# Kernel optimization log

Hardware: AMD Instinct MI355X
Metric: run time of the kernel (lower is better)

The kernel has to match this reference:

```python
import jax, jax.numpy as jnp
import numpy as np
from jax import lax

D_MODEL = 768
N_LAYER = 4
VOCAB = 50280  # 50277 padded to multiple of 8
D_INNER = 2 * D_MODEL
D_STATE = 16
D_CONV = 4
DT_RANK = 48  # ceil(768/16)
EPS = 1e-5


def setup_inputs() -> dict:
    key = jax.random.key(0)
    ks = iter(jax.random.split(key, 16))
    s = 0.02
    B, L = 1, 1024
    inp = {
        "input_ids": jax.random.randint(next(ks), (B, L), 0, 50277, dtype=jnp.int64).astype(jnp.int32),
        "embedding": jax.random.normal(next(ks), (VOCAB, D_MODEL), jnp.float32) * s,
        "in_proj_w": jax.random.normal(next(ks), (N_LAYER, 2 * D_INNER, D_MODEL), jnp.float32) * s,
        "conv_w": jax.random.normal(next(ks), (N_LAYER, D_INNER, 1, D_CONV), jnp.float32) * s,
        "conv_b": jnp.zeros((N_LAYER, D_INNER), jnp.float32),
        "x_proj_w": jax.random.normal(next(ks), (N_LAYER, DT_RANK + 2 * D_STATE, D_INNER), jnp.float32) * s,
        "dt_proj_w": jax.random.normal(next(ks), (N_LAYER, D_INNER, DT_RANK), jnp.float32) * s,
        "dt_proj_b": jax.random.uniform(next(ks), (N_LAYER, D_INNER), jnp.float32, -4.0, -2.0),
        "A_log": jnp.log(jnp.broadcast_to(jnp.arange(1, D_STATE + 1, dtype=jnp.float32), (N_LAYER, D_INNER, D_STATE))),
        "D_param": jnp.ones((N_LAYER, D_INNER), jnp.float32),
        "out_proj_w": jax.random.normal(next(ks), (N_LAYER, D_MODEL, D_INNER), jnp.float32) * s,
        "norm_w": jnp.ones((N_LAYER, D_MODEL), jnp.float32),
        "norm_f_w": jnp.ones((D_MODEL,), jnp.float32),
    }
    return inp


def rmsnorm(x, w):
    var = jnp.mean(jnp.square(x), axis=-1, keepdims=True)
    return x * lax.rsqrt(var + EPS) * w


def silu(x):
    return x * jax.nn.sigmoid(x)


def mamba_mixer(h, in_w, cw, cb, xw, dtw, dtb, A_log, Dp, ow):
    B, L, _ = h.shape
    xz = jnp.einsum("bld,ed->ble", h, in_w)          # [B,L,2*d_inner]
    x, z = jnp.split(xz, 2, axis=-1)
    # causal depthwise conv1d over length
    xc = lax.conv_general_dilated(
        x.transpose(0, 2, 1), cw, (1,), [(D_CONV - 1, 0)],
        dimension_numbers=("NCH", "OIH", "NCH"), feature_group_count=D_INNER,
    ).transpose(0, 2, 1) + cb                          # [B,L,d_inner]
    xc = silu(xc)
    dbl = jnp.einsum("bld,ed->ble", xc, xw)            # [B,L,R+2N]
    dt = jax.nn.softplus(jnp.einsum("blr,dr->bld", dbl[..., :DT_RANK], dtw) + dtb)
    Bm = dbl[..., DT_RANK:DT_RANK + D_STATE]           # [B,L,N]
    Cm = dbl[..., DT_RANK + D_STATE:]                  # [B,L,N]
    A = -jnp.exp(A_log)                                # [d_inner,N]
    dA = jnp.exp(dt[..., None] * A)                    # [B,L,d_inner,N]
    dBx = dt[..., None] * Bm[:, :, None, :] * xc[..., None]

    def step(s, inp):
        a, b, c = inp
        s = a * s + b
        y = jnp.einsum("bdn,bn->bd", s, c)
        return s, y

    s0 = jnp.zeros((B, D_INNER, D_STATE), h.dtype)
    _, ys = lax.scan(step, s0, (dA.transpose(1, 0, 2, 3), dBx.transpose(1, 0, 2, 3), Cm.transpose(1, 0, 2)))
    y = ys.transpose(1, 0, 2) + xc * Dp                # [B,L,d_inner]
    y = y * silu(z)
    return jnp.einsum("ble,de->bld", y, ow)


def reference(input_ids, embedding, in_proj_w, conv_w, conv_b, x_proj_w,
              dt_proj_w, dt_proj_b, A_log, D_param, out_proj_w, norm_w, norm_f_w):
    h = embedding[input_ids]                           # [B,L,D]
    for i in range(N_LAYER):
        h = h + mamba_mixer(rmsnorm(h, norm_w[i]), in_proj_w[i], conv_w[i], conv_b[i],
                            x_proj_w[i], dt_proj_w[i], dt_proj_b[i], A_log[i],
                            D_param[i], out_proj_w[i])
    h = rmsnorm(h, norm_f_w)
    logits = jnp.einsum("bld,vd->blv", h, embedding)   # tied lm_head
    return logits
```

## Files before the change

### kernel.cpp

```cpp
#include <hip/hip_runtime.h>
#include <cstdint>
#include <cstddef>

#define N_LAYER 4
#define VOCABSZ 50280
#define VOCABPAD 50304
#define DMODEL 768
#define DINNER 1536
#define DSTATE 16
#define DTRANK 48
#define SEQL 1024

typedef __bf16 bf16x8 __attribute__((ext_vector_type(8)));
typedef unsigned short us8 __attribute__((ext_vector_type(8)));
typedef float f32x4 __attribute__((ext_vector_type(4)));

__device__ __forceinline__ unsigned short f2bf(float f) {
    unsigned int u = __builtin_bit_cast(unsigned int, f);
    u = (u + 0x7FFFu + ((u >> 16) & 1u)) >> 16;
    return (unsigned short)u;
}

__device__ __forceinline__ void glds16(const unsigned short* g, unsigned short* l) {
    __builtin_amdgcn_global_load_lds(
        (const __attribute__((address_space(1))) void*)g,
        (__attribute__((address_space(3))) void*)l, 16, 0, 0);
}

__global__ __launch_bounds__(256) void cvt_bf16_kernel(
    const float* __restrict__ src, unsigned short* __restrict__ dst, int n8)
{
    int i = blockIdx.x * 256 + threadIdx.x;
    if (i >= n8) return;
    const float4* s = (const float4*)src + (size_t)i * 2;
    float4 a = s[0], b = s[1];
    us8 o = { f2bf(a.x), f2bf(a.y), f2bf(a.z), f2bf(a.w),
              f2bf(b.x), f2bf(b.y), f2bf(b.z), f2bf(b.w) };
    *(us8*)(dst + (size_t)i * 8) = o;
}

__global__ __launch_bounds__(256) void cvt_xw_kernel(
    const float* __restrict__ xw, unsigned short* __restrict__ xwB)
{
    int g = blockIdx.x * 256 + threadIdx.x;
    if (g >= N_LAYER * 128 * 192) return;
    int row = g / 192;
    int c8  = g % 192;
    int layer = row >> 7;
    int r = row & 127;
    us8 o;
    if (r < 80) {
        const float4* s = (const float4*)(xw + ((size_t)(layer * 80 + r) * DINNER) + c8 * 8);
        float4 a = s[0], b = s[1];
        o = (us8){ f2bf(a.x), f2bf(a.y), f2bf(a.z), f2bf(a.w),
                   f2bf(b.x), f2bf(b.y), f2bf(b.z), f2bf(b.w) };
    } else {
        o = (us8){0, 0, 0, 0, 0, 0, 0, 0};
    }
    *(us8*)(xwB + (size_t)row * DINNER + c8 * 8) = o;
}

template <int ADD>
__device__ __forceinline__ void gemm_bf_body(
    const unsigned short* __restrict__ A, const unsigned short* __restrict__ B,
    const float* __restrict__ ADDSRC, float* __restrict__ C, int N, int K)
{
    __shared__ unsigned short sA[128 * 32];
    __shared__ unsigned short sB[128 * 32];

    const int tid  = threadIdx.x;
    const int lane = tid & 63;
    const int wave = tid >> 6;
    const int wm = (wave & 1) * 64;
    const int wn = (wave >> 1) * 64;
    const int bid = blockIdx.x;
    const int cpx = (int)gridDim.x >> 3;
    const int swz = (bid & 7) * cpx + (bid >> 3);
    const int bm = (swz & 7) << 7;
    const int bn = (swz >> 3) << 7;

    const unsigned short* Ag0 = A + (size_t)(bm + (tid >> 2)) * K + (tid & 3) * 8;
    const unsigned short* Ag1 = Ag0 + (size_t)64 * K;
    const unsigned short* Bg0 = B + (size_t)(bn + (tid >> 2)) * K + (tid & 3) * 8;
    const unsigned short* Bg1 = Bg0 + (size_t)64 * K;
    unsigned short* lA0 = sA + tid * 8;
    unsigned short* lA1 = lA0 + 2048;
    unsigned short* lB0 = sB + tid * 8;
    unsigned short* lB1 = lB0 + 2048;

    f32x4 acc[4][4];
#pragma unroll
    for (int i = 0; i < 4; ++i)
#pragma unroll
        for (int j = 0; j < 4; ++j) acc[i][j] = (f32x4){0.f, 0.f, 0.f, 0.f};

    const int fr = (lane & 15) * 32 + (lane >> 4) * 8;

    for (int k0 = 0; k0 < K; k0 += 32) {
        __syncthreads();
        glds16(Ag0, lA0);
        glds16(Ag1, lA1);
        glds16(Bg0, lB0);
        glds16(Bg1, lB1);
        Ag0 += 32; Ag1 += 32; Bg0 += 32; Bg1 += 32;
        __syncthreads();

        bf16x8 af[4], bfr[4];
#pragma unroll
        for (int t = 0; t < 4; ++t) {
            af[t]  = __builtin_bit_cast(bf16x8, *(const us8*)&sA[(wm + t * 16) * 32 + fr]);
            bfr[t] = __builtin_bit_cast(bf16x8, *(const us8*)&sB[(wn + t * 16) * 32 + fr]);
        }
#pragma unroll
        for (int mt = 0; mt < 4; ++mt)
#pragma unroll
            for (int nt = 0; nt < 4; ++nt)
                acc[mt][nt] = __builtin_amdgcn_mfma_f32_16x16x32_bf16(
                    af[mt], bfr[nt], acc[mt][nt], 0, 0, 0);
    }

    const int cn = lane & 15;
    const int cm = (lane >> 4) * 4;
#pragma unroll
    for (int mt = 0; mt < 4; ++mt) {
#pragma unroll
        for (int nt = 0; nt < 4; ++nt) {
            int n = bn + wn + nt * 16 + cn;
            if (n < N) {
#pragma unroll
                for (int r = 0; r < 4; ++r) {
                    int m = bm + wm + mt * 16 + cm + r;
                    size_t idx = (size_t)m * N + n;
                    float v = acc[mt][nt][r];
                    if constexpr (ADD) v += ADDSRC[idx];
                    C[idx] = v;
                }
            }
        }
    }
}

__global__ __launch_bounds__(256) void gemm_in_kernel(
    const unsigned short* __restrict__ A, const unsigned short* __restrict__ B,
    float* __restrict__ C, int N, int K)
{ gemm_bf_body<0>(A, B, nullptr, C, N, K); }

__global__ __launch_bounds__(256) void gemm_out_kernel(
    const unsigned short* __restrict__ A, const unsigned short* __restrict__ B,
    const float* __restrict__ ADDSRC, float* __restrict__ C, int N, int K)
{ gemm_bf_body<1>(A, B, ADDSRC, C, N, K); }

__global__ __launch_bounds__(256) void gemm_xproj_kernel(
    const unsigned short* __restrict__ A, const unsigned short* __restrict__ B,
    float* __restrict__ C, int N, int K)
{ gemm_bf_body<0>(A, B, nullptr, C, N, K); }

__global__ __launch_bounds__(256) void gemm_logits_kernel(
    const unsigned short* __restrict__ A, const unsigned short* __restrict__ B,
    float* __restrict__ C, int N, int K)
{ gemm_bf_body<0>(A, B, nullptr, C, N, K); }

template <int ADD>
__global__ __launch_bounds__(256) void gemm_fb_kernel(
    const float* __restrict__ A, const float* __restrict__ B,
    const float* __restrict__ ADDSRC, float* __restrict__ C,
    int N, int K)
{
    __shared__ unsigned short sA[128 * 40];
    __shared__ unsigned short sB[128 * 40];
    const int tid  = threadIdx.x;
    const int lane = tid & 63;
    const int wave = tid >> 6;
    const int wm = (wave & 1) * 64;
    const int wn = (wave >> 1) * 64;
    const int bm = blockIdx.y * 128;
    const int bn = blockIdx.x * 128;
    const int srow = tid >> 1;
    const int scol = (tid & 1) * 16;
    const float* Ap = A + (size_t)(bm + srow) * K + scol;
    const int brow  = bn + srow;
    const bool bvalid = brow < N;
    const float* Bp = B + (size_t)(bvalid ? brow : 0) * K + scol;
    f32x4 acc[4][4];
#pragma unroll
    for (int i = 0; i < 4; ++i)
#pragma unroll
        for (int j = 0; j < 4; ++j) acc[i][j] = (f32x4){0.f, 0.f, 0.f, 0.f};
    unsigned short* sAp = &sA[srow * 40 + scol];
    unsigned short* sBp = &sB[srow * 40 + scol];
    const int fr = (lane & 15) * 40 + (lane >> 4) * 8;
    for (int k0 = 0; k0 < K; k0 += 32) {
        float4 a0 = *(const float4*)(Ap + k0);
        float4 a1 = *(const float4*)(Ap + k0 + 4);
        float4 a2 = *(const float4*)(Ap + k0 + 8);
        float4 a3 = *(const float4*)(Ap + k0 + 12);
        float4 b0, b1, b2, b3;
        if (bvalid) {
            b0 = *(const float4*)(Bp + k0);
            b1 = *(const float4*)(Bp + k0 + 4);
            b2 = *(const float4*)(Bp + k0 + 8);
            b3 = *(const float4*)(Bp + k0 + 12);
        } else {
            b0 = make_float4(0.f, 0.f, 0.f, 0.f);
            b1 = b0; b2 = b0; b3 = b0;
        }
        __syncthreads();
        us8 va0 = { f2bf(a0.x), f2bf(a0.y), f2bf(a0.z), f2bf(a0.w),
                    f2bf(a1.x), f2bf(a1.y), f2bf(a1.z), f2bf(a1.w) };
        us8 va1 = { f2bf(a2.x), f2bf(a2.y), f2bf(a2.z), f2bf(a2.w),
                    f2bf(a3.x), f2bf(a3.y), f2bf(a3.z), f2bf(a3.w) };
        us8 vb0 = { f2bf(b0.x), f2bf(b0.y), f2bf(b0.z), f2bf(b0.w),
                    f2bf(b1.x), f2bf(b1.y), f2bf(b1.z), f2bf(b1.w) };
        us8 vb1 = { f2bf(b2.x), f2bf(b2.y), f2bf(b2.z), f2bf(b2.w),
                    f2bf(b3.x), f2bf(b3.y), f2bf(b3.z), f2bf(b3.w) };
        *(us8*)(sAp)     = va0;
        *(us8*)(sAp + 8) = va1;
        *(us8*)(sBp)     = vb0;
        *(us8*)(sBp + 8) = vb1;
        __syncthreads();
        bf16x8 af[4], bfr[4];
#pragma unroll
        for (int t = 0; t < 4; ++t) {
            af[t]  = __builtin_bit_cast(bf16x8, *(const us8*)&sA[wm * 40 + t * 640 + fr]);
            bfr[t] = __builtin_bit_cast(bf16x8, *(const us8*)&sB[wn * 40 + t * 640 + fr]);
        }
#pragma unroll
        for (int mt = 0; mt < 4; ++mt)
#pragma unroll
            for (int nt = 0; nt < 4; ++nt)
                acc[mt][nt] = __builtin_amdgcn_mfma_f32_16x16x32_bf16(
                    af[mt], bfr[nt], acc[mt][nt], 0, 0, 0);
    }
    const int cn = lane & 15;
    const int cm = (lane >> 4) * 4;
#pragma unroll
    for (int mt = 0; mt < 4; ++mt) {
#pragma unroll
        for (int nt = 0; nt < 4; ++nt) {
            int n = bn + wn + nt * 16 + cn;
            if (n < N) {
#pragma unroll
                for (int r = 0; r < 4; ++r) {
                    int m = bm + wm + mt * 16 + cm + r;
                    size_t idx = (size_t)m * N + n;
                    float v = acc[mt][nt][r];
                    if constexpr (ADD) v += ADDSRC[idx];
                    C[idx] = v;
                }
            }
        }
    }
}

__global__ __launch_bounds__(256) void embed_kernel(
    const int* __restrict__ ids, const float* __restrict__ emb, float* __restrict__ h)
{
    int l = blockIdx.x;
    int id = ids[l];
    const float* src = emb + (size_t)id * DMODEL;
    for (int d = threadIdx.x; d < DMODEL; d += 256) h[(size_t)l * DMODEL + d] = src[d];
}

template <typename OT>
__global__ __launch_bounds__(256) void rmsnorm_kernel(
    const float* __restrict__ x, const float* __restrict__ w,
    OT* __restrict__ out, int D)
{
    int l = blockIdx.x;
    const float* xr = x + (size_t)l * D;
    float ss = 0.f;
    for (int d = threadIdx.x; d < D; d += 256) { float v = xr[d]; ss += v * v; }
#pragma unroll
    for (int off = 32; off > 0; off >>= 1) ss += __shfl_down(ss, off, 64);
    __shared__ float red[4];
    __shared__ float invs;
    if ((threadIdx.x & 63) == 0) red[threadIdx.x >> 6] = ss;
    __syncthreads();
    if (threadIdx.x == 0)
        invs = rsqrtf((red[0] + red[1] + red[2] + red[3]) / (float)D + 1e-5f);
    __syncthreads();
    float inv = invs;
    for (int d = threadIdx.x; d < D; d += 256) {
        float v = xr[d] * inv * w[d];
        if constexpr (sizeof(OT) == 2) out[(size_t)l * D + d] = f2bf(v);
        else                           out[(size_t)l * D + d] = v;
    }
}

__global__ __launch_bounds__(256) void conv_silu_kernel(
    const float* __restrict__ xz, const float* __restrict__ cw,
    const float* __restrict__ cb, float* __restrict__ xc,
    unsigned short* __restrict__ xcB)
{
    int l = blockIdx.x / 6;
    int d = (blockIdx.x % 6) * 256 + threadIdx.x;
    float w0 = cw[d * 4], w1 = cw[d * 4 + 1], w2 = cw[d * 4 + 2], w3 = cw[d * 4 + 3];
    float acc = cb[d];
    if (l >= 3) acc += xz[(size_t)(l - 3) * 3072 + d] * w0;
    if (l >= 2) acc += xz[(size_t)(l - 2) * 3072 + d] * w1;
    if (l >= 1) acc += xz[(size_t)(l - 1) * 3072 + d] * w2;
    acc += xz[(size_t)l * 3072 + d] * w3;
    float sig = 1.f / (1.f + __expf(-acc));
    float v = acc * sig;
    size_t idx = (size_t)l * DINNER + d;
    xc[idx]  = v;
    xcB[idx] = f2bf(v);
}

__global__ __launch_bounds__(256) void xproj_kernel(
    const float* __restrict__ xc, const float* __restrict__ xw, float* __restrict__ dbl)
{
    int l = blockIdx.x;
    __shared__ float sx[DINNER];
    for (int d = threadIdx.x; d < DINNER; d += 256) sx[d] = xc[(size_t)l * DINNER + d];
    __syncthreads();
    int wave = threadIdx.x >> 6, lane = threadIdx.x & 63;
    for (int e = wave * 20; e < wave * 20 + 20; ++e) {
        const float* wr = xw + (size_t)e * DINNER;
        float s = 0.f;
        for (int d = lane; d < DINNER; d += 64) s += sx[d] * wr[d];
#pragma unroll
        for (int off = 32; off > 0; off >>= 1) s += __shfl_down(s, off, 64);
        if (lane == 0) dbl[l * 80 + e] = s;
    }
}

__global__ __launch_bounds__(256) void dtproj_kernel(
    const float* __restrict__ dbl, const float* __restrict__ dtw,
    const float* __restrict__ dtb, float* __restrict__ dt)
{
    int l = blockIdx.x / 6;
    int e = (blockIdx.x % 6) * 256 + threadIdx.x;
    __shared__ float sd[48];
    if (threadIdx.x < 48) sd[threadIdx.x] = dbl[l * 80 + threadIdx.x];
    __syncthreads();
    float a = dtb[e];
    const float4* wr = (const float4*)(dtw + (size_t)e * 48);
#pragma unroll
    for (int q = 0; q < 12; ++q) {
        float4 w4 = wr[q];
        a += sd[q * 4] * w4.x + sd[q * 4 + 1] * w4.y + sd[q * 4 + 2] * w4.z + sd[q * 4 + 3] * w4.w;
    }
    dt[(size_t)l * DINNER + e] = (a > 20.f) ? a : log1pf(__expf(a));
}

template <typename OT>
__global__ __launch_bounds__(64) void scan_kernel(
    const float* __restrict__ dt, const float* __restrict__ dbl,
    const float* __restrict__ xc, const float* __restrict__ xz,
    const float* __restrict__ alog, const float* __restrict__ dpar,
    OT* __restrict__ yf)
{
    int d0 = blockIdx.x * 4;
    int lane = threadIdx.x;
    int n = lane & 15;
    int dloc = lane >> 4;
    int d = d0 + dloc;
    float A = -__expf(alog[d * 16 + n]);
    float Dq[4];
#pragma unroll
    for (int q = 0; q < 4; ++q) Dq[q] = dpar[d0 + q];

    __shared__ float sdt[64][4];
    __shared__ float sxc[64][4];
    __shared__ float sz[64][4];
    __shared__ float sB[64][16];
    __shared__ float sC[64][16];
    __shared__ float pp[4][64][17];

    float s = 0.f;
    for (int c0 = 0; c0 < SEQL; c0 += 64) {
        int l = c0 + lane;
        *(float4*)&sdt[lane][0] = *(const float4*)&dt[(size_t)l * DINNER + d0];
        *(float4*)&sxc[lane][0] = *(const float4*)&xc[(size_t)l * DINNER + d0];
        *(float4*)&sz[lane][0]  = *(const float4*)&xz[(size_t)l * 3072 + DINNER + d0];
#pragma unroll
        for (int q = 0; q < 4; ++q) {
            *(float4*)&sB[lane][q * 4] = *(const float4*)&dbl[l * 80 + 48 + q * 4];
            *(float4*)&sC[lane][q * 4] = *(const float4*)&dbl[l * 80 + 64 + q * 4];
        }
        __syncthreads();
#pragma unroll 4
        for (int j = 0; j < 64; ++j) {
            float dtv = sdt[j][dloc];
            float xv  = sxc[j][dloc];
            float a = __expf(dtv * A);
            s = fmaf(a, s, dtv * sB[j][n] * xv);
            pp[dloc][j][n] = s * sC[j][n];
        }
        __syncthreads();
#pragma unroll
        for (int q = 0; q < 4; ++q) {
            float accv = 0.f;
#pragma unroll
            for (int nn = 0; nn < 16; ++nn) accv += pp[q][lane][nn];
            float xv = sxc[lane][q];
            float zv = sz[lane][q];
            float sig = 1.f / (1.f + __expf(-zv));
            float v = (accv + xv * Dq[q]) * (zv * sig);
            if constexpr (sizeof(OT) == 2) yf[(size_t)(c0 + lane) * DINNER + d0 + q] = f2bf(v);
            else                           yf[(size_t)(c0 + lane) * DINNER + d0 + q] = v;
        }
        __syncthreads();
    }
}

extern "C" void kernel_launch(void* const* d_in, const int* in_sizes, int n_in,
                              void* d_out, int out_size, void* d_ws, size_t ws_size,
                              hipStream_t stream)
{
    const int*   ids  = (const int*)d_in[0];
    const float* emb  = (const float*)d_in[1];
    const float* inw  = (const float*)d_in[2];
    const float* cw   = (const float*)d_in[3];
    const float* cb   = (const float*)d_in[4];
    const float* xw   = (const float*)d_in[5];
    const float* dtw  = (const float*)d_in[6];
    const float* dtb  = (const float*)d_in[7];
    const float* alog = (const float*)d_in[8];
    const float* dpar = (const float*)d_in[9];
    const float* ow   = (const float*)d_in[10];
    const float* nw   = (const float*)d_in[11];
    const float* nfw  = (const float*)d_in[12];
    float* out = (float*)d_out;

    const size_t MAIN_WS = 138936320ull;

    if (ws_size >= MAIN_WS) {
        char* p = (char*)d_ws;
        float* h    = (float*)p;                 p += (size_t)SEQL * DMODEL * 4;
        float* xz   = (float*)p;                 p += (size_t)SEQL * 3072 * 4;
        float* xc   = (float*)p;                 p += (size_t)SEQL * DINNER * 4;
        float* dbl  = (float*)p;                 p += (size_t)SEQL * 80 * 4;
        float* dt   = (float*)p;                 p += (size_t)SEQL * DINNER * 4;
        unsigned short* xnB  = (unsigned short*)p; p += (size_t)SEQL * DMODEL * 2;
        unsigned short* yfB  = (unsigned short*)p; p += (size_t)SEQL * DINNER * 2;
        unsigned short* embB = (unsigned short*)p; p += (size_t)VOCABPAD * DMODEL * 2;
        unsigned short* inwB = (unsigned short*)p; p += (size_t)N_LAYER * 3072 * DMODEL * 2;
        unsigned short* owB  = (unsigned short*)p; p += (size_t)N_LAYER * DMODEL * DINNER * 2;

        unsigned short* xwB = (unsigned short*)out;
        unsigned short* xcB = xwB + (size_t)N_LAYER * 128 * DINNER;

        int n8;
        n8 = VOCABSZ * DMODEL / 8;
        cvt_bf16_kernel<<<(n8 + 255) / 256, 256, 0, stream>>>(emb, embB, n8);
        n8 = N_LAYER * 3072 * DMODEL / 8;
        cvt_bf16_kernel<<<(n8 + 255) / 256, 256, 0, stream>>>(inw, inwB, n8);
        n8 = N_LAYER * DMODEL * DINNER / 8;
        cvt_bf16_kernel<<<(n8 + 255) / 256, 256, 0, stream>>>(ow, owB, n8);
        cvt_xw_kernel<<<(N_LAYER * 128 * 192 + 255) / 256, 256, 0, stream>>>(xw, xwB);

        embed_kernel<<<SEQL, 256, 0, stream>>>(ids, emb, h);

        for (int i = 0; i < N_LAYER; ++i) {
            rmsnorm_kernel<unsigned short><<<SEQL, 256, 0, stream>>>(
                h, nw + (size_t)i * DMODEL, xnB, DMODEL);
            gemm_in_kernel<<<8 * (3072 / 128), 256, 0, stream>>>(
                xnB, inwB + (size_t)i * 3072 * DMODEL, xz, 3072, DMODEL);
            conv_silu_kernel<<<SEQL * 6, 256, 0, stream>>>(
                xz, cw + (size_t)i * DINNER * 4, cb + (size_t)i * DINNER, xc, xcB);
            gemm_xproj_kernel<<<8, 256, 0, stream>>>(
                xcB, xwB + (size_t)i * 128 * DINNER, dbl, 80, DINNER);
            dtproj_kernel<<<SEQL * 6, 256, 0, stream>>>(
                dbl, dtw + (size_t)i * DINNER * DTRANK, dtb + (size_t)i * DINNER, dt);
            scan_kernel<unsigned short><<<DINNER / 4, 64, 0, stream>>>(
                dt, dbl, xc, xz, alog + (size_t)i * DINNER * DSTATE,
                dpar + (size_t)i * DINNER, yfB);
            gemm_out_kernel<<<8 * (DMODEL / 128), 256, 0, stream>>>(
                yfB, owB + (size_t)i * DMODEL * DINNER, h, h, DMODEL, DINNER);
        }

        rmsnorm_kernel<unsigned short><<<SEQL, 256, 0, stream>>>(h, nfw, xnB, DMODEL);
        gemm_logits_kernel<<<8 * ((VOCABSZ + 127) / 128), 256, 0, stream>>>(
            xnB, embB, out, VOCABSZ, DMODEL);
    } else {
        float* h   = (float*)d_ws;
        float* xn  = h  + (size_t)SEQL * DMODEL;
        float* xz  = xn + (size_t)SEQL * DMODEL;
        float* xc  = xz + (size_t)SEQL * 3072;
        float* dbl = xc + (size_t)SEQL * DINNER;
        float* dt  = dbl + (size_t)SEQL * 80;
        float* yf  = dt + (size_t)SEQL * DINNER;
        unsigned short* xcB = (unsigned short*)out;

        embed_kernel<<<SEQL, 256, 0, stream>>>(ids, emb, h);
        for (int i = 0; i < N_LAYER; ++i) {
            rmsnorm_kernel<float><<<SEQL, 256, 0, stream>>>(h, nw + (size_t)i * DMODEL, xn, DMODEL);
            gemm_fb_kernel<0><<<dim3(3072 / 128, SEQL / 128), 256, 0, stream>>>(
                xn, inw + (size_t)i * 3072 * DMODEL, nullptr, xz, 3072, DMODEL);
            conv_silu_kernel<<<SEQL * 6, 256, 0, stream>>>(
                xz, cw + (size_t)i * DINNER * 4, cb + (size_t)i * DINNER, xc, xcB);
            xproj_kernel<<<SEQL, 256, 0, stream>>>(xc, xw + (size_t)i * 80 * DINNER, dbl);
            dtproj_kernel<<<SEQL * 6, 256, 0, stream>>>(
                dbl, dtw + (size_t)i * DINNER * DTRANK, dtb + (size_t)i * DINNER, dt);
            scan_kernel<float><<<DINNER / 4, 64, 0, stream>>>(
                dt, dbl, xc, xz, alog + (size_t)i * DINNER * DSTATE, dpar + (size_t)i * DINNER, yf);
            gemm_fb_kernel<1><<<dim3(DMODEL / 128, SEQL / 128), 256, 0, stream>>>(
                yf, ow + (size_t)i * DMODEL * DINNER, h, h, DMODEL, DINNER);
        }
        rmsnorm_kernel<float><<<SEQL, 256, 0, stream>>>(h, nfw, xn, DMODEL);
        gemm_fb_kernel<0><<<dim3((VOCABSZ + 127) / 128, SEQL / 128), 256, 0, stream>>>(
            xn, emb, nullptr, out, VOCABSZ, DMODEL);
    }
}
```

Before: 1.291 ms.

## Double-buffer LDS tiles in bf16 GEMM and XOR-swizzle layout against bank conflicts

The bf16 MFMA GEMM now keeps two LDS buffers per operand, so the global-to-LDS loads for the next K-slice are issued before the MFMAs on the current slice run. This cuts the barrier count per K step and hides load latency. The column chunk each thread loads is also XOR-swizzled by row, and fragment reads apply the matching swizzle, to reduce LDS bank conflicts. LDS use doubles, which may lower occupancy, and the loop assumes K is a multiple of 64.

```diff
diff --git a/kernel.cpp b/kernel.cpp
--- a/kernel.cpp
+++ b/kernel.cpp
@@ -60,13 +60,33 @@
     *(us8*)(xwB + (size_t)row * DINNER + c8 * 8) = o;
 }
 
+__device__ __forceinline__ void gemm_compute32(
+    const unsigned short* sAbuf, const unsigned short* sBbuf,
+    int wm, int wn, int frs, f32x4 (&acc)[4][4])
+{
+    bf16x8 af[4], bfr[4];
+#pragma unroll
+    for (int t = 0; t < 4; ++t) {
+        af[t]  = __builtin_bit_cast(bf16x8, *(const us8*)&sAbuf[(wm + t * 16) * 32 + frs]);
+        bfr[t] = __builtin_bit_cast(bf16x8, *(const us8*)&sBbuf[(wn + t * 16) * 32 + frs]);
+    }
+#pragma unroll
+    for (int mt = 0; mt < 4; ++mt)
+#pragma unroll
+        for (int nt = 0; nt < 4; ++nt)
+            acc[mt][nt] = __builtin_amdgcn_mfma_f32_16x16x32_bf16(
+                af[mt], bfr[nt], acc[mt][nt], 0, 0, 0);
+}
+
 template <int ADD>
 __device__ __forceinline__ void gemm_bf_body(
     const unsigned short* __restrict__ A, const unsigned short* __restrict__ B,
     const float* __restrict__ ADDSRC, float* __restrict__ C, int N, int K)
 {
-    __shared__ unsigned short sA[128 * 32];
-    __shared__ unsigned short sB[128 * 32];
+    __shared__ unsigned short sA0[128 * 32];
+    __shared__ unsigned short sA1[128 * 32];
+    __shared__ unsigned short sB0[128 * 32];
+    __shared__ unsigned short sB1[128 * 32];
 
     const int tid  = threadIdx.x;
     const int lane = tid & 63;
@@ -79,14 +99,15 @@
     const int bm = (swz & 7) << 7;
     const int bn = (swz >> 3) << 7;
 
-    const unsigned short* Ag0 = A + (size_t)(bm + (tid >> 2)) * K + (tid & 3) * 8;
+    const int scol = ((tid & 3) ^ ((tid >> 3) & 3)) * 8;
+    const unsigned short* Ag0 = A + (size_t)(bm + (tid >> 2)) * K + scol;
     const unsigned short* Ag1 = Ag0 + (size_t)64 * K;
-    const unsigned short* Bg0 = B + (size_t)(bn + (tid >> 2)) * K + (tid & 3) * 8;
+    const unsigned short* Bg0 = B + (size_t)(bn + (tid >> 2)) * K + scol;
     const unsigned short* Bg1 = Bg0 + (size_t)64 * K;
-    unsigned short* lA0 = sA + tid * 8;
-    unsigned short* lA1 = lA0 + 2048;
-    unsigned short* lB0 = sB + tid * 8;
-    unsigned short* lB1 = lB0 + 2048;
+    unsigned short* lA0a = sA0 + tid * 8;  unsigned short* lA0b = lA0a + 2048;
+    unsigned short* lA1a = sA1 + tid * 8;  unsigned short* lA1b = lA1a + 2048;
+    unsigned short* lB0a = sB0 + tid * 8;  unsigned short* lB0b = lB0a + 2048;
+    unsigned short* lB1a = sB1 + tid * 8;  unsigned short* lB1b = lB1a + 2048;
 
     f32x4 acc[4][4];
 #pragma unroll
@@ -94,29 +115,27 @@
 #pragma unroll
         for (int j = 0; j < 4; ++j) acc[i][j] = (f32x4){0.f, 0.f, 0.f, 0.f};
 
-    const int fr = (lane & 15) * 32 + (lane >> 4) * 8;
-
-    for (int k0 = 0; k0 < K; k0 += 32) {
-        __syncthreads();
-        glds16(Ag0, lA0);
-        glds16(Ag1, lA1);
-        glds16(Bg0, lB0);
-        glds16(Bg1, lB1);
+    const int frs = (lane & 15) * 32 + (((lane >> 4) ^ ((lane >> 1) & 3))) * 8;
+
+    glds16(Ag0, lA0a); glds16(Ag1, lA0b);
+    glds16(Bg0, lB0a); glds16(Bg1, lB0b);
+    Ag0 += 32; Ag1 += 32; Bg0 += 32; Bg1 += 32;
+    __syncthreads();
+
+    for (int k0 = 0; k0 < K; k0 += 64) {
+        glds16(Ag0, lA1a); glds16(Ag1, lA1b);
+        glds16(Bg0, lB1a); glds16(Bg1, lB1b);
         Ag0 += 32; Ag1 += 32; Bg0 += 32; Bg1 += 32;
-        __syncthreads();
-
-        bf16x8 af[4], bfr[4];
-#pragma unroll
-        for (int t = 0; t < 4; ++t) {
-            af[t]  = __builtin_bit_cast(bf16x8, *(const us8*)&sA[(wm + t * 16) * 32 + fr]);
-            bfr[t] = __builtin_bit_cast(bf16x8, *(const us8*)&sB[(wn + t * 16) * 32 + fr]);
-        }
-#pragma unroll
-        for (int mt = 0; mt < 4; ++mt)
-#pragma unroll
-            for (int nt = 0; nt < 4; ++nt)
-                acc[mt][nt] = __builtin_amdgcn_mfma_f32_16x16x32_bf16(
-                    af[mt], bfr[nt], acc[mt][nt], 0, 0, 0);
+        gemm_compute32(sA0, sB0, wm, wn, frs, acc);
+        __syncthreads();
+
+        if (k0 + 64 < K) {
+            glds16(Ag0, lA0a); glds16(Ag1, lA0b);
+            glds16(Bg0, lB0a); glds16(Bg1, lB0b);
+            Ag0 += 32; Ag1 += 32; Bg0 += 32; Bg1 += 32;
+        }
+        gemm_compute32(sA1, sB1, wm, wn, frs, acc);
+        __syncthreads();
     }
 
     const int cn = lane & 15;
```

New measurement: 1.221 ms. 5.5% less time.
